# Optimization experiments

Measured on AMD Instinct MI355X. Metric: run time of the kernel, lower is better.

## Reference

```python
import jax, jax.numpy as jnp
import numpy as np
import math

EPS_NORM = 1e-6
EPS_COS = 1e-6


def _rms_norm(x, scale, eps):
    ms = jnp.mean(jnp.square(x), axis=-1, keepdims=True)
    return x * (scale * jax.lax.rsqrt(ms + eps))


def _apply_rope(x, theta):
    # x: [n, nh, s, e], theta: [n, nh, s, d] with 2*d <= e
    d = theta.shape[-1]
    x1, x2, rest = x[..., :d], x[..., d:2 * d], x[..., 2 * d:]
    cos, sin = jnp.cos(theta), jnp.sin(theta)
    y1 = x1 * cos - x2 * sin
    y2 = x2 * cos + x1 * sin
    return jnp.concatenate([y1, y2, rest], axis=-1)


def _make_freqs(d_head, n_heads):
    dim = d_head // 2
    log_min, log_max = math.log(math.pi), math.log(10.0 * math.pi)
    f = np.exp(np.linspace(log_min, log_max, n_heads * dim // 4 + 1, dtype=np.float64)[:-1])
    return jnp.asarray(f.reshape(dim // 4, n_heads).T, dtype=jnp.float32)  # [n_heads, dim//4]


def setup_inputs() -> dict:
    key = jax.random.key(0)
    ks = jax.random.split(key, 8)
    n, H, W, d_model = 4, 32, 32, 1024
    d_head, n_heads, cond_f = 64, 16, 1024
    x = jax.random.normal(ks[0], (n, H, W, d_model), dtype=jnp.float32)
    pos = jax.random.uniform(ks[1], (n, H, W, 2), dtype=jnp.float32) * 2.0 - 1.0
    cond = jax.random.normal(ks[2], (n, cond_f), dtype=jnp.float32)
    norm_scale = jnp.ones((d_model,), dtype=jnp.float32)
    ada_w = jax.random.normal(ks[3], (3 * d_model, cond_f), dtype=jnp.float32) * 0.02
    ada_b = jnp.zeros((3 * d_model,), dtype=jnp.float32)
    qkv_w = jax.random.normal(ks[4], (3 * d_model, d_model), dtype=jnp.float32) * 0.02
    attn_scale = jnp.full((n_heads,), 10.0, dtype=jnp.float32)
    out_w = jax.random.normal(ks[5], (d_model, d_model), dtype=jnp.float32) * 0.02
    freqs = _make_freqs(d_head, n_heads)
    return {"x": x, "pos": pos, "cond": cond, "norm_scale": norm_scale,
            "ada_w": ada_w, "ada_b": ada_b, "qkv_w": qkv_w,
            "attn_scale": attn_scale, "out_w": out_w, "freqs": freqs}


def reference(x, pos, cond, norm_scale, ada_w, ada_b, qkv_w, attn_scale, out_w, freqs):
    n, H, W, d_model = x.shape
    n_heads, nf = freqs.shape          # nf = d_head//4... actually (d_head//2)//4
    d_head = d_model // n_heads
    s = H * W
    skip = x
    # adaLN modulation
    mod = jax.nn.silu(cond) @ ada_w.T + ada_b              # [n, 3*d_model]
    shift, scale, gate = jnp.split(mod, 3, axis=-1)        # each [n, d_model]
    xn = _rms_norm(x, norm_scale, EPS_NORM)
    xm = xn * (1.0 + scale[:, None, None, :]) + shift[:, None, None, :]
    # qkv projection: layout (t nh e) on last dim
    qkv = (xm @ qkv_w.T).reshape(n, s, 3, n_heads, d_head)
    q, k, v = qkv[:, :, 0], qkv[:, :, 1], qkv[:, :, 2]     # [n, s, nh, e]
    q = jnp.transpose(q, (0, 2, 1, 3))                     # [n, nh, s, e]
    k = jnp.transpose(k, (0, 2, 1, 3))
    v = jnp.transpose(v, (0, 2, 1, 3))
    # cosine-sim scaling per head
    sqrt_scale = jnp.sqrt(attn_scale)[None, :, None, None]
    q = q * (sqrt_scale * jax.lax.rsqrt(jnp.sum(jnp.square(q), axis=-1, keepdims=True) + EPS_COS))
    k = k * (sqrt_scale * jax.lax.rsqrt(jnp.sum(jnp.square(k), axis=-1, keepdims=True) + EPS_COS))
    # axial RoPE angles
    posf = pos.reshape(n, s, 2)
    theta_h = posf[:, :, None, 0:1] * freqs                # [n, s, nh, nf]
    theta_w = posf[:, :, None, 1:2] * freqs
    theta = jnp.concatenate([theta_h, theta_w], axis=-1)   # [n, s, nh, 2*nf]
    theta = jnp.transpose(theta, (0, 2, 1, 3))             # [n, nh, s, 2*nf]
    q = _apply_rope(q, theta)
    k = _apply_rope(k, theta)
    # attention with softmax scale 1.0 (cosine-sim already scaled)
    scores = jnp.einsum('bnse,bnte->bnst', q, k)
    attn = jax.nn.softmax(scores, axis=-1)
    o = jnp.einsum('bnst,bnte->bnse', attn, v)             # [n, nh, s, e]
    o = jnp.transpose(o, (0, 2, 1, 3)).reshape(n, H, W, d_model)
    o = o @ out_w.T
    return skip + gate[:, None, None, :] * o
```

## Files before the change

kernel.cpp:

```cpp
#include <hip/hip_runtime.h>
#include <stdint.h>

typedef __bf16 bf16x8 __attribute__((ext_vector_type(8)));
typedef uint16_t u16x8 __attribute__((ext_vector_type(8)));
typedef float f32x4 __attribute__((ext_vector_type(4)));

#define DEV static __device__ __forceinline__

DEV uint16_t f2bf(float f) {
  union { float f; uint32_t u; } v; v.f = f;
  return (uint16_t)((v.u + 0x8000u) >> 16);
}
DEV float bf2f(uint16_t h) {
  union { uint32_t u; float f; } v; v.u = ((uint32_t)h) << 16;
  return v.f;
}

#define GLOAD_LDS16(g, l)                                                     \
  __builtin_amdgcn_global_load_lds(                                           \
      (__attribute__((address_space(1))) void*)(g),                           \
      (__attribute__((address_space(3))) void*)(l), 16, 0, 0)

__global__ void k_conv(const float* __restrict__ src, uint16_t* __restrict__ dst, int n) {
  int i = blockIdx.x * blockDim.x + threadIdx.x;
  int stride = gridDim.x * blockDim.x;
  for (; i < n; i += stride) dst[i] = f2bf(src[i]);
}

__global__ void k_mod(const float* __restrict__ cond, const float* __restrict__ ada_w,
                      const float* __restrict__ ada_b, float* __restrict__ mod) {
  int w = threadIdx.x >> 6, lane = threadIdx.x & 63;
  int gid = blockIdx.x * 4 + w;
  int b = gid / 3072, j = gid - b * 3072;
  const float* cw = cond + b * 1024;
  const float* aw = ada_w + (size_t)j * 1024;
  float sum = 0.f;
  for (int i = 0; i < 16; ++i) {
    int f = lane + (i << 6);
    float c = cw[f];
    float sc = c / (1.f + __expf(-c));
    sum += sc * aw[f];
  }
  for (int m = 32; m; m >>= 1) sum += __shfl_xor(sum, m, 64);
  if (lane == 0) mod[b * 3072 + j] = sum + ada_b[j];
}

__global__ void k_norm_mod(const float* __restrict__ x, const float* __restrict__ norm_scale,
                           const float* __restrict__ mod, uint16_t* __restrict__ xm) {
  int row = blockIdx.x;
  int b = row >> 10;
  const float* xr = x + (size_t)row * 1024;
  const float* shiftp = mod + b * 3072;
  const float* scalep = shiftp + 1024;
  int t = threadIdx.x;
  float v[4];
  float s = 0.f;
  for (int i = 0; i < 4; ++i) { v[i] = xr[t + (i << 8)]; s += v[i] * v[i]; }
  for (int m = 32; m; m >>= 1) s += __shfl_xor(s, m, 64);
  __shared__ float red[4];
  if ((t & 63) == 0) red[t >> 6] = s;
  __syncthreads();
  s = red[0] + red[1] + red[2] + red[3];
  float inv = rsqrtf(s * (1.f / 1024.f) + 1e-6f);
  uint16_t* xo = xm + (size_t)row * 1024;
  for (int i = 0; i < 4; ++i) {
    int c = t + (i << 8);
    float val = v[i] * inv * norm_scale[c];
    val = val * (1.f + scalep[c]) + shiftp[c];
    xo[c] = f2bf(val);
  }
}

template <int N, int EPI>
__global__ __launch_bounds__(256) void k_gemm(const uint16_t* __restrict__ A,
                                              const uint16_t* __restrict__ B,
                                              uint16_t* __restrict__ Cbf,
                                              const float* __restrict__ skip,
                                              const float* __restrict__ modp,
                                              float* __restrict__ Cout) {
  constexpr int K = 1024;
  __shared__ uint16_t As[128 * 32];
  __shared__ uint16_t Bs[128 * 32];
  int t = threadIdx.x;
  int lane = t & 63;
  int w = t >> 6, wr = w >> 1, wc = w & 1;
  int bm = blockIdx.y, bn = blockIdx.x;
  f32x4 acc[4][4] = {};
  const size_t a_base = (size_t)(bm * 128) * K;
  const size_t b_base = (size_t)(bn * 128) * K;
  int r = t >> 2, cch = t & 3;
  for (int kt = 0; kt < K / 32; ++kt) {
    __syncthreads();
#pragma unroll
    for (int i = 0; i < 2; ++i) {
      int rr = r + (i << 6);
      int cs = (cch ^ ((rr >> 1) & 3)) << 3;
      GLOAD_LDS16(A + a_base + (size_t)rr * K + kt * 32 + cs, As + rr * 32 + (cch << 3));
      GLOAD_LDS16(B + b_base + (size_t)rr * K + kt * 32 + cs, Bs + rr * 32 + (cch << 3));
    }
    __syncthreads();
    bf16x8 af[4], bfr[4];
    int lq = lane >> 4;
#pragma unroll
    for (int m = 0; m < 4; ++m) {
      int R = wr * 64 + m * 16 + (lane & 15);
      af[m] = *reinterpret_cast<const bf16x8*>(&As[R * 32 + ((lq ^ ((R >> 1) & 3)) << 3)]);
    }
#pragma unroll
    for (int n = 0; n < 4; ++n) {
      int R = wc * 64 + n * 16 + (lane & 15);
      bfr[n] = *reinterpret_cast<const bf16x8*>(&Bs[R * 32 + ((lq ^ ((R >> 1) & 3)) << 3)]);
    }
#pragma unroll
    for (int m = 0; m < 4; ++m)
#pragma unroll
      for (int n = 0; n < 4; ++n)
        acc[m][n] = __builtin_amdgcn_mfma_f32_16x16x32_bf16(af[m], bfr[n], acc[m][n], 0, 0, 0);
  }
  int row0 = bm * 128 + wr * 64;
  int col0 = bn * 128 + wc * 64;
#pragma unroll
  for (int m = 0; m < 4; ++m)
#pragma unroll
    for (int n = 0; n < 4; ++n)
#pragma unroll
      for (int rr = 0; rr < 4; ++rr) {
        int R = row0 + m * 16 + ((lane >> 4) << 2) + rr;
        int C = col0 + n * 16 + (lane & 15);
        float v = acc[m][n][rr];
        if (EPI == 0) {
          Cbf[(size_t)R * N + C] = f2bf(v);
        } else {
          float g = modp[(R >> 10) * 3072 + 2048 + C];
          Cout[(size_t)R * N + C] = skip[(size_t)R * N + C] + g * v;
        }
      }
}

__global__ __launch_bounds__(256) void k_qkvpost(
    const uint16_t* __restrict__ qkv, const float* __restrict__ pos,
    const float* __restrict__ freqs, const float* __restrict__ attn_scale,
    uint16_t* __restrict__ Qb, uint16_t* __restrict__ Kb, uint16_t* __restrict__ Vt) {
  __shared__ uint16_t vtile[64 * 66];
  int t = threadIdx.x;
  int st = blockIdx.x, bh = blockIdx.y;
  int b = bh >> 4, h = bh & 15;
  int r = t >> 2;
  int s = t & 3;
  int sp = st * 64 + r;
  size_t m = (size_t)b * 1024 + sp;
  const uint16_t* basep = qkv + m * 3072 + h * 64 + s * 16;
  bf16x8 q0 = *reinterpret_cast<const bf16x8*>(basep);
  bf16x8 q1 = *reinterpret_cast<const bf16x8*>(basep + 8);
  bf16x8 k0 = *reinterpret_cast<const bf16x8*>(basep + 1024);
  bf16x8 k1 = *reinterpret_cast<const bf16x8*>(basep + 1032);
  u16x8 v0 = *reinterpret_cast<const u16x8*>(basep + 2048);
  u16x8 v1 = *reinterpret_cast<const u16x8*>(basep + 2056);
  float qv[16], kv[16];
#pragma unroll
  for (int i = 0; i < 8; ++i) {
    qv[i] = (float)q0[i]; qv[8 + i] = (float)q1[i];
    kv[i] = (float)k0[i]; kv[8 + i] = (float)k1[i];
  }
  float sq = 0.f, sk = 0.f;
#pragma unroll
  for (int i = 0; i < 16; ++i) { sq += qv[i] * qv[i]; sk += kv[i] * kv[i]; }
  sq += __shfl_xor(sq, 1, 64); sq += __shfl_xor(sq, 2, 64);
  sk += __shfl_xor(sk, 1, 64); sk += __shfl_xor(sk, 2, 64);
  float ss = sqrtf(attn_scale[h]);
  float qs = ss * rsqrtf(sq + 1e-6f);
  float ks = ss * rsqrtf(sk + 1e-6f);
#pragma unroll
  for (int i = 0; i < 16; ++i) { qv[i] *= qs; kv[i] *= ks; }
  float p0 = pos[m * 2], p1 = pos[m * 2 + 1];
  float sgn = (s == 0) ? -1.f : 1.f;
#pragma unroll
  for (int i = 0; i < 16; ++i) {
    float pq = __shfl_xor(qv[i], 1, 64);
    float pk = __shfl_xor(kv[i], 1, 64);
    if (s < 2) {
      float th = ((i < 8) ? p0 : p1) * freqs[h * 8 + (i & 7)];
      float sn, cs;
      __sincosf(th, &sn, &cs);
      qv[i] = qv[i] * cs + sgn * pq * sn;
      kv[i] = kv[i] * cs + sgn * pk * sn;
    }
  }
  bf16x8 qo0, qo1, ko0, ko1;
#pragma unroll
  for (int i = 0; i < 8; ++i) {
    qo0[i] = (__bf16)qv[i]; qo1[i] = (__bf16)qv[8 + i];
    ko0[i] = (__bf16)kv[i]; ko1[i] = (__bf16)kv[8 + i];
  }
  size_t qkb = ((size_t)bh * 1024 + sp) * 64 + s * 16;
  *reinterpret_cast<bf16x8*>(Qb + qkb) = qo0;
  *reinterpret_cast<bf16x8*>(Qb + qkb + 8) = qo1;
  *reinterpret_cast<bf16x8*>(Kb + qkb) = ko0;
  *reinterpret_cast<bf16x8*>(Kb + qkb + 8) = ko1;
#pragma unroll
  for (int i = 0; i < 8; ++i) {
    vtile[(s * 16 + i) * 66 + r] = v0[i];
    vtile[(s * 16 + 8 + i) * 66 + r] = v1[i];
  }
  __syncthreads();
  int d = t >> 2, c = t & 3;
  u16x8 w0, w1;
#pragma unroll
  for (int i = 0; i < 8; ++i) {
    w0[i] = vtile[d * 66 + c * 16 + i];
    w1[i] = vtile[d * 66 + c * 16 + 8 + i];
  }
  size_t vb = ((size_t)bh * 64 + d) * 1024 + st * 64 + c * 16;
  *reinterpret_cast<u16x8*>(Vt + vb) = w0;
  *reinterpret_cast<u16x8*>(Vt + vb + 8) = w1;
}

__global__ __launch_bounds__(256) void k_attn(const uint16_t* __restrict__ Qb,
                                              const uint16_t* __restrict__ Kb,
                                              const uint16_t* __restrict__ Vt,
                                              uint16_t* __restrict__ obuf) {
  __shared__ uint16_t Ks[64 * 64];
  __shared__ uint16_t Vs[64 * 64];
  __shared__ uint16_t Ps[4][32 * 88];
  int t = threadIdx.x, lane = t & 63, w = t >> 6;
  int qt = blockIdx.y, bh = blockIdx.x;
  int b = bh >> 4, h = bh & 15;
  int klo = (lane >> 4) << 3;
  bf16x8 qf[2][2];
#pragma unroll
  for (int qs = 0; qs < 2; ++qs) {
    int qrow = qt * 128 + w * 32 + qs * 16 + (lane & 15);
    const uint16_t* qptr = Qb + ((size_t)bh * 1024 + qrow) * 64 + klo;
    qf[qs][0] = *reinterpret_cast<const bf16x8*>(qptr);
    qf[qs][1] = *reinterpret_cast<const bf16x8*>(qptr + 32);
  }
  f32x4 oacc[2][4] = {};
  float denom[2][4] = {};
  const size_t kbase = (size_t)bh * 1024 * 64;
  const size_t vbase = (size_t)bh * 64 * 1024;
  for (int kt = 0; kt < 16; ++kt) {
    __syncthreads();
#pragma unroll
    for (int i = 0; i < 2; ++i) {
      int slot = t + (i << 8);
      int row = slot >> 3;
      int ce = ((slot & 7) ^ (row & 7)) << 3;
      GLOAD_LDS16(Kb + kbase + (size_t)(kt * 64 + row) * 64 + ce, Ks + slot * 8);
      GLOAD_LDS16(Vt + vbase + (size_t)row * 1024 + kt * 64 + ce, Vs + slot * 8);
    }
    __syncthreads();
    f32x4 s[2][4];
#pragma unroll
    for (int n = 0; n < 4; ++n) {
      int row = n * 16 + (lane & 15);
      int sw = (row & 7) << 3;
      bf16x8 kf0 = *reinterpret_cast<const bf16x8*>(&Ks[row * 64 + (klo ^ sw)]);
      bf16x8 kf1 = *reinterpret_cast<const bf16x8*>(&Ks[row * 64 + ((32 + klo) ^ sw)]);
#pragma unroll
      for (int qs = 0; qs < 2; ++qs) {
        f32x4 z = {};
        z = __builtin_amdgcn_mfma_f32_16x16x32_bf16(qf[qs][0], kf0, z, 0, 0, 0);
        z = __builtin_amdgcn_mfma_f32_16x16x32_bf16(qf[qs][1], kf1, z, 0, 0, 0);
        s[qs][n] = z;
      }
    }
#pragma unroll
    for (int qs = 0; qs < 2; ++qs)
#pragma unroll
      for (int n = 0; n < 4; ++n)
#pragma unroll
        for (int rr = 0; rr < 4; ++rr) {
          float p = __expf(s[qs][n][rr]);
          denom[qs][rr] += p;
          Ps[w][(qs * 16 + ((lane >> 4) << 2) + rr) * 88 + n * 16 + (lane & 15)] = f2bf(p);
        }
    bf16x8 pa[2][2];
#pragma unroll
    for (int qs = 0; qs < 2; ++qs) {
      pa[qs][0] = *reinterpret_cast<const bf16x8*>(&Ps[w][(qs * 16 + (lane & 15)) * 88 + klo]);
      pa[qs][1] = *reinterpret_cast<const bf16x8*>(&Ps[w][(qs * 16 + (lane & 15)) * 88 + 32 + klo]);
    }
#pragma unroll
    for (int dt = 0; dt < 4; ++dt) {
      int row = dt * 16 + (lane & 15);
      int sw = (row & 7) << 3;
      bf16x8 vf0 = *reinterpret_cast<const bf16x8*>(&Vs[row * 64 + (klo ^ sw)]);
      bf16x8 vf1 = *reinterpret_cast<const bf16x8*>(&Vs[row * 64 + ((32 + klo) ^ sw)]);
#pragma unroll
      for (int qs = 0; qs < 2; ++qs) {
        oacc[qs][dt] = __builtin_amdgcn_mfma_f32_16x16x32_bf16(pa[qs][0], vf0, oacc[qs][dt], 0, 0, 0);
        oacc[qs][dt] = __builtin_amdgcn_mfma_f32_16x16x32_bf16(pa[qs][1], vf1, oacc[qs][dt], 0, 0, 0);
      }
    }
  }
#pragma unroll
  for (int qs = 0; qs < 2; ++qs)
#pragma unroll
    for (int rr = 0; rr < 4; ++rr)
      for (int msk = 8; msk; msk >>= 1) denom[qs][rr] += __shfl_xor(denom[qs][rr], msk, 64);
#pragma unroll
  for (int qs = 0; qs < 2; ++qs)
#pragma unroll
    for (int rr = 0; rr < 4; ++rr) {
      float rinv = 1.f / denom[qs][rr];
      int sp = qt * 128 + w * 32 + qs * 16 + ((lane >> 4) << 2) + rr;
      size_t orow = ((size_t)b * 1024 + sp) * 1024 + h * 64;
#pragma unroll
      for (int dt = 0; dt < 4; ++dt)
        obuf[orow + dt * 16 + (lane & 15)] = f2bf(oacc[qs][dt][rr] * rinv);
    }
}

extern "C" void kernel_launch(void* const* d_in, const int* in_sizes, int n_in,
                              void* d_out, int out_size, void* d_ws, size_t ws_size,
                              hipStream_t stream) {
  const float* x = (const float*)d_in[0];
  const float* pos = (const float*)d_in[1];
  const float* cond = (const float*)d_in[2];
  const float* norm_scale = (const float*)d_in[3];
  const float* ada_w = (const float*)d_in[4];
  const float* ada_b = (const float*)d_in[5];
  const float* qkv_w = (const float*)d_in[6];
  const float* attn_scale = (const float*)d_in[7];
  const float* out_w = (const float*)d_in[8];
  const float* freqs = (const float*)d_in[9];
  float* out = (float*)d_out;
  char* ws = (char*)d_ws;
  float* mod = (float*)(ws + 0);
  uint16_t* xm = (uint16_t*)(ws + 65536);
  uint16_t* qkvw_bf = (uint16_t*)(ws + 8454144);
  uint16_t* outw_bf = (uint16_t*)(ws + 14745600);
  uint16_t* qkv = (uint16_t*)(ws + 16842752);
  uint16_t* Qb = (uint16_t*)(ws + 42008576);
  uint16_t* Kb = (uint16_t*)(ws + 50397184);
  uint16_t* Vt = (uint16_t*)(ws + 58785792);
  uint16_t* obuf = (uint16_t*)(ws + 67174400);

  k_conv<<<dim3(1024), dim3(256), 0, stream>>>(qkv_w, qkvw_bf, 3 * 1024 * 1024);
  k_conv<<<dim3(512), dim3(256), 0, stream>>>(out_w, outw_bf, 1024 * 1024);
  k_mod<<<dim3(3072), dim3(256), 0, stream>>>(cond, ada_w, ada_b, mod);
  k_norm_mod<<<dim3(4096), dim3(256), 0, stream>>>(x, norm_scale, mod, xm);
  k_gemm<3072, 0><<<dim3(24, 32), dim3(256), 0, stream>>>(xm, qkvw_bf, qkv, nullptr, nullptr, nullptr);
  k_qkvpost<<<dim3(16, 64), dim3(256), 0, stream>>>(qkv, pos, freqs, attn_scale, Qb, Kb, Vt);
  k_attn<<<dim3(64, 8), dim3(256), 0, stream>>>(Qb, Kb, Vt, obuf);
  k_gemm<1024, 1><<<dim3(8, 32), dim3(256), 0, stream>>>(obuf, outw_bf, nullptr, x, mod, out);
}
```

Baseline: 124.8 us.

## Fuse QKV post-processing (cosine norm, RoPE, V transpose) into QKV GEMM epilogue

The QKV projection GEMM now applies per-head cosine normalization and axial RoPE to Q/K directly from accumulator registers and writes them in head-major layout. V tiles are transposed through the reused LDS tiles before being written. This removes the intermediate bf16 qkv buffer round-trip and one kernel launch. The cost is a heavier GEMM epilogue with scattered 2-byte stores for Q/K and extra barriers.

```diff
diff --git a/kernel.cpp b/kernel.cpp
--- a/kernel.cpp
+++ b/kernel.cpp
@@ -71,6 +71,123 @@
   }
 }
 
+__global__ __launch_bounds__(256) void k_gemmqkv(
+    const uint16_t* __restrict__ A, const uint16_t* __restrict__ B,
+    const float* __restrict__ pos, const float* __restrict__ attn_scale,
+    const float* __restrict__ freqs, uint16_t* __restrict__ Qb,
+    uint16_t* __restrict__ Kb, uint16_t* __restrict__ Vt) {
+  constexpr int K = 1024;
+  __shared__ uint16_t As[128 * 32];
+  __shared__ uint16_t Bs[128 * 32];
+  int t = threadIdx.x;
+  int lane = t & 63;
+  int w = t >> 6, wr = w >> 1, wc = w & 1;
+  int bm = blockIdx.y, bn = blockIdx.x;
+  f32x4 acc[4][4] = {};
+  const size_t a_base = (size_t)(bm * 128) * K;
+  const size_t b_base = (size_t)(bn * 128) * K;
+  int r = t >> 2, cch = t & 3;
+  for (int kt = 0; kt < K / 32; ++kt) {
+    __syncthreads();
+#pragma unroll
+    for (int i = 0; i < 2; ++i) {
+      int rr = r + (i << 6);
+      int cs = (cch ^ ((rr >> 1) & 3)) << 3;
+      GLOAD_LDS16(A + a_base + (size_t)rr * K + kt * 32 + cs, As + rr * 32 + (cch << 3));
+      GLOAD_LDS16(B + b_base + (size_t)rr * K + kt * 32 + cs, Bs + rr * 32 + (cch << 3));
+    }
+    __syncthreads();
+    bf16x8 af[4], bfr[4];
+    int lq = lane >> 4;
+#pragma unroll
+    for (int m = 0; m < 4; ++m) {
+      int R = wr * 64 + m * 16 + (lane & 15);
+      af[m] = *reinterpret_cast<const bf16x8*>(&As[R * 32 + ((lq ^ ((R >> 1) & 3)) << 3)]);
+    }
+#pragma unroll
+    for (int n = 0; n < 4; ++n) {
+      int R = wc * 64 + n * 16 + (lane & 15);
+      bfr[n] = *reinterpret_cast<const bf16x8*>(&Bs[R * 32 + ((lq ^ ((R >> 1) & 3)) << 3)]);
+    }
+#pragma unroll
+    for (int m = 0; m < 4; ++m)
+#pragma unroll
+      for (int n = 0; n < 4; ++n)
+        acc[m][n] = __builtin_amdgcn_mfma_f32_16x16x32_bf16(af[m], bfr[n], acc[m][n], 0, 0, 0);
+  }
+  int c = bn * 2 + wc;
+  int sec = c >> 4;
+  int h = c & 15;
+  int i = lane & 15, g = lane >> 4;
+  int row0 = bm * 128 + wr * 64;
+  __syncthreads();
+  if (sec < 2) {
+    uint16_t* dst = sec ? Kb : Qb;
+    float ss = sqrtf(attn_scale[h]);
+#pragma unroll
+    for (int m = 0; m < 4; ++m)
+#pragma unroll
+      for (int rr = 0; rr < 4; ++rr) {
+        int R = row0 + m * 16 + g * 4 + rr;
+        float v0 = acc[m][0][rr], v1 = acc[m][1][rr];
+        float v2 = acc[m][2][rr], v3 = acc[m][3][rr];
+        float p = v0 * v0 + v1 * v1 + v2 * v2 + v3 * v3;
+        p += __shfl_xor(p, 1, 64); p += __shfl_xor(p, 2, 64);
+        p += __shfl_xor(p, 4, 64); p += __shfl_xor(p, 8, 64);
+        float sc = ss * rsqrtf(p + 1e-6f);
+        v0 *= sc; v1 *= sc; v2 *= sc; v3 *= sc;
+        float th = ((i < 8) ? pos[2 * R] : pos[2 * R + 1]) * freqs[h * 8 + (i & 7)];
+        float sn, csn;
+        __sincosf(th, &sn, &csn);
+        float y0 = v0 * csn - v1 * sn;
+        float y1 = v1 * csn + v0 * sn;
+        size_t base = (((size_t)((R >> 10) * 16 + h)) * 1024 + (R & 1023)) * 64 + i;
+        dst[base] = f2bf(y0);
+        dst[base + 16] = f2bf(y1);
+        dst[base + 32] = f2bf(v2);
+        dst[base + 48] = f2bf(v3);
+      }
+    __syncthreads();
+    __syncthreads();
+    __syncthreads();
+    __syncthreads();
+  } else {
+    uint16_t* vt = wc ? Bs : As;
+    int b = row0 >> 10, spbase = row0 & 1023;
+    size_t vrow = ((size_t)(b * 16 + h)) * 64;
+#pragma unroll
+    for (int rnd = 0; rnd < 2; ++rnd) {
+      if (wr == rnd) {
+#pragma unroll
+        for (int m = 0; m < 4; ++m)
+#pragma unroll
+          for (int n = 0; n < 4; ++n)
+#pragma unroll
+            for (int rr = 0; rr < 4; ++rr) {
+              int sl = m * 16 + g * 4 + rr;
+              int d = n * 16 + i;
+              vt[d * 64 + (sl ^ ((d & 7) << 3))] = f2bf(acc[m][n][rr]);
+            }
+      }
+      __syncthreads();
+      if (wr == rnd) {
+#pragma unroll
+        for (int p = 0; p < 4; ++p) {
+          int d = p * 16 + (lane >> 2);
+          int s0 = (lane & 3) * 16;
+          int xr = (d & 7) << 3;
+          u16x8 va = *reinterpret_cast<const u16x8*>(&vt[d * 64 + (s0 ^ xr)]);
+          u16x8 vb = *reinterpret_cast<const u16x8*>(&vt[d * 64 + ((s0 + 8) ^ xr)]);
+          size_t o = (vrow + d) * 1024 + spbase + s0;
+          *reinterpret_cast<u16x8*>(Vt + o) = va;
+          *reinterpret_cast<u16x8*>(Vt + o + 8) = vb;
+        }
+      }
+      __syncthreads();
+    }
+  }
+}
+
 template <int N, int EPI>
 __global__ __launch_bounds__(256) void k_gemm(const uint16_t* __restrict__ A,
                                               const uint16_t* __restrict__ B,
@@ -137,84 +254,6 @@
       }
 }
 
-__global__ __launch_bounds__(256) void k_qkvpost(
-    const uint16_t* __restrict__ qkv, const float* __restrict__ pos,
-    const float* __restrict__ freqs, const float* __restrict__ attn_scale,
-    uint16_t* __restrict__ Qb, uint16_t* __restrict__ Kb, uint16_t* __restrict__ Vt) {
-  __shared__ uint16_t vtile[64 * 66];
-  int t = threadIdx.x;
-  int st = blockIdx.x, bh = blockIdx.y;
-  int b = bh >> 4, h = bh & 15;
-  int r = t >> 2;
-  int s = t & 3;
-  int sp = st * 64 + r;
-  size_t m = (size_t)b * 1024 + sp;
-  const uint16_t* basep = qkv + m * 3072 + h * 64 + s * 16;
-  bf16x8 q0 = *reinterpret_cast<const bf16x8*>(basep);
-  bf16x8 q1 = *reinterpret_cast<const bf16x8*>(basep + 8);
-  bf16x8 k0 = *reinterpret_cast<const bf16x8*>(basep + 1024);
-  bf16x8 k1 = *reinterpret_cast<const bf16x8*>(basep + 1032);
-  u16x8 v0 = *reinterpret_cast<const u16x8*>(basep + 2048);
-  u16x8 v1 = *reinterpret_cast<const u16x8*>(basep + 2056);
-  float qv[16], kv[16];
-#pragma unroll
-  for (int i = 0; i < 8; ++i) {
-    qv[i] = (float)q0[i]; qv[8 + i] = (float)q1[i];
-    kv[i] = (float)k0[i]; kv[8 + i] = (float)k1[i];
-  }
-  float sq = 0.f, sk = 0.f;
-#pragma unroll
-  for (int i = 0; i < 16; ++i) { sq += qv[i] * qv[i]; sk += kv[i] * kv[i]; }
-  sq += __shfl_xor(sq, 1, 64); sq += __shfl_xor(sq, 2, 64);
-  sk += __shfl_xor(sk, 1, 64); sk += __shfl_xor(sk, 2, 64);
-  float ss = sqrtf(attn_scale[h]);
-  float qs = ss * rsqrtf(sq + 1e-6f);
-  float ks = ss * rsqrtf(sk + 1e-6f);
-#pragma unroll
-  for (int i = 0; i < 16; ++i) { qv[i] *= qs; kv[i] *= ks; }
-  float p0 = pos[m * 2], p1 = pos[m * 2 + 1];
-  float sgn = (s == 0) ? -1.f : 1.f;
-#pragma unroll
-  for (int i = 0; i < 16; ++i) {
-    float pq = __shfl_xor(qv[i], 1, 64);
-    float pk = __shfl_xor(kv[i], 1, 64);
-    if (s < 2) {
-      float th = ((i < 8) ? p0 : p1) * freqs[h * 8 + (i & 7)];
-      float sn, cs;
-      __sincosf(th, &sn, &cs);
-      qv[i] = qv[i] * cs + sgn * pq * sn;
-      kv[i] = kv[i] * cs + sgn * pk * sn;
-    }
-  }
-  bf16x8 qo0, qo1, ko0, ko1;
-#pragma unroll
-  for (int i = 0; i < 8; ++i) {
-    qo0[i] = (__bf16)qv[i]; qo1[i] = (__bf16)qv[8 + i];
-    ko0[i] = (__bf16)kv[i]; ko1[i] = (__bf16)kv[8 + i];
-  }
-  size_t qkb = ((size_t)bh * 1024 + sp) * 64 + s * 16;
-  *reinterpret_cast<bf16x8*>(Qb + qkb) = qo0;
-  *reinterpret_cast<bf16x8*>(Qb + qkb + 8) = qo1;
-  *reinterpret_cast<bf16x8*>(Kb + qkb) = ko0;
-  *reinterpret_cast<bf16x8*>(Kb + qkb + 8) = ko1;
-#pragma unroll
-  for (int i = 0; i < 8; ++i) {
-    vtile[(s * 16 + i) * 66 + r] = v0[i];
-    vtile[(s * 16 + 8 + i) * 66 + r] = v1[i];
-  }
-  __syncthreads();
-  int d = t >> 2, c = t & 3;
-  u16x8 w0, w1;
-#pragma unroll
-  for (int i = 0; i < 8; ++i) {
-    w0[i] = vtile[d * 66 + c * 16 + i];
-    w1[i] = vtile[d * 66 + c * 16 + 8 + i];
-  }
-  size_t vb = ((size_t)bh * 64 + d) * 1024 + st * 64 + c * 16;
-  *reinterpret_cast<u16x8*>(Vt + vb) = w0;
-  *reinterpret_cast<u16x8*>(Vt + vb + 8) = w1;
-}
-
 __global__ __launch_bounds__(256) void k_attn(const uint16_t* __restrict__ Qb,
                                               const uint16_t* __restrict__ Kb,
                                               const uint16_t* __restrict__ Vt,
@@ -330,7 +369,6 @@
   uint16_t* xm = (uint16_t*)(ws + 65536);
   uint16_t* qkvw_bf = (uint16_t*)(ws + 8454144);
   uint16_t* outw_bf = (uint16_t*)(ws + 14745600);
-  uint16_t* qkv = (uint16_t*)(ws + 16842752);
   uint16_t* Qb = (uint16_t*)(ws + 42008576);
   uint16_t* Kb = (uint16_t*)(ws + 50397184);
   uint16_t* Vt = (uint16_t*)(ws + 58785792);
@@ -340,8 +378,7 @@
   k_conv<<<dim3(512), dim3(256), 0, stream>>>(out_w, outw_bf, 1024 * 1024);
   k_mod<<<dim3(3072), dim3(256), 0, stream>>>(cond, ada_w, ada_b, mod);
   k_norm_mod<<<dim3(4096), dim3(256), 0, stream>>>(x, norm_scale, mod, xm);
-  k_gemm<3072, 0><<<dim3(24, 32), dim3(256), 0, stream>>>(xm, qkvw_bf, qkv, nullptr, nullptr, nullptr);
-  k_qkvpost<<<dim3(16, 64), dim3(256), 0, stream>>>(qkv, pos, freqs, attn_scale, Qb, Kb, Vt);
+  k_gemmqkv<<<dim3(24, 32), dim3(256), 0, stream>>>(xm, qkvw_bf, pos, attn_scale, freqs, Qb, Kb, Vt);
   k_attn<<<dim3(64, 8), dim3(256), 0, stream>>>(Qb, Kb, Vt, obuf);
   k_gemm<1024, 1><<<dim3(8, 32), dim3(256), 0, stream>>>(obuf, outw_bf, nullptr, x, mod, out);
 }
```

Result: no change. 125.7 us (+0.7%).
